# Kernel tuning notes

Measured on AMD Instinct MI355X. Metric: run time of the kernel, lower is better.

## Reference

```python
import jax, jax.numpy as jnp
import numpy as np

DIM = 512
HEADS = 8
HEAD_DIM = DIM // HEADS
SCALE = HEAD_DIM ** -0.5
GROUP1 = np.array([2, 3, 5, 6, 1, 4, 0, 7, 8, 9, 14, 15, 11, 12, 10, 13])
GROUP2 = np.array([0, 1, 2, 3, 5, 6, 4, 7])
EPS = 1e-5


def setup_inputs() -> dict:
    key = jax.random.key(0)
    ks = jax.random.split(key, 6)
    B, N, C = 4096, 16, DIM
    x = jax.random.normal(ks[0], (B, N, C), dtype=jnp.float32)
    w_q = jax.random.normal(ks[1], (C, C), dtype=jnp.float32) * 0.02
    w_kv = jax.random.normal(ks[2], (2 * C, C), dtype=jnp.float32) * 0.02
    w_proj = jax.random.normal(ks[3], (C, C), dtype=jnp.float32) * 0.02
    b_proj = jax.random.normal(ks[4], (C,), dtype=jnp.float32) * 0.02
    gamma = jnp.ones((C,), dtype=jnp.float32)
    beta = jnp.zeros((C,), dtype=jnp.float32)
    return {"x": x, "w_q": w_q, "w_kv": w_kv, "w_proj": w_proj,
            "b_proj": b_proj, "gamma": gamma, "beta": beta}


def _layernorm(x, gamma, beta):
    mu = jnp.mean(x, axis=-1, keepdims=True)
    var = jnp.mean(jnp.square(x - mu), axis=-1, keepdims=True)
    return (x - mu) * jax.lax.rsqrt(var + EPS) * gamma + beta


def _avg_pool_pairs(x):
    # x: (B, L, C) -> (B, L//2, C), AvgPool1d(kernel=2, stride=2) over L
    return 0.5 * (x[:, 0::2] + x[:, 1::2])


def reference(x, w_q, w_kv, w_proj, b_proj, gamma, beta):
    B, N, C = x.shape
    q = (x @ w_q.T).reshape(B, N, HEADS, HEAD_DIM).transpose(0, 2, 1, 3)  # (B,H,N,d)
    # gather + avgpool preprocessing
    p1 = _avg_pool_pairs(x[:, GROUP1])  # (B, 8, C)
    p2 = _avg_pool_pairs(x[:, GROUP2])  # (B, 4, C)
    pools = jnp.concatenate([x, p1, p2], axis=1)  # (B, N+12, C)
    pools = _layernorm(pools, gamma, beta)
    M = pools.shape[1]
    kv = (pools @ w_kv.T).reshape(B, M, 2, HEADS, HEAD_DIM).transpose(2, 0, 3, 1, 4)
    k, v = kv[0], kv[1]  # (B,H,M,d)
    attn = jax.nn.softmax(jnp.einsum('bhnd,bhmd->bhnm', q, k) * SCALE, axis=-1)
    out = jnp.einsum('bhnm,bhmd->bhnd', attn, v)  # (B,H,N,d)
    out = out.transpose(0, 2, 1, 3).reshape(B, N, C)
    return out @ w_proj.T + b_proj
```

## Files before the change

kernel.cpp:

```cpp
#include <hip/hip_runtime.h>
#include <hip/hip_bf16.h>
#include <cstdint>
#include <cstddef>


using bf16 = __hip_bfloat16;

#define B_SZ   4096
#define NTOK   16
#define CDIM   512
#define MPOOL  28
#define NHEAD  8
#define HDIM   64
#define LN_EPS 1e-5f
#define ATT_SCALE 0.125f

typedef short bf16x8 __attribute__((ext_vector_type(8)));
typedef float f32x4  __attribute__((ext_vector_type(4)));

__constant__ int c_g1[16] = {2,3,5,6,1,4,0,7,8,9,14,15,11,12,10,13};
__constant__ int c_g2[8]  = {0,1,2,3,5,6,4,7};

__device__ __forceinline__ unsigned short f2b(float f) {
    unsigned u = __float_as_uint(f);
    return (unsigned short)((u + 0x7FFFu + ((u >> 16) & 1u)) >> 16);
}

__device__ __forceinline__ void lds_cp16(const void* g, void* l) {
    __builtin_amdgcn_global_load_lds(
        (const __attribute__((address_space(1))) void*)g,
        (__attribute__((address_space(3))) void*)l, 16, 0, 0);
}

__global__ __launch_bounds__(256) void f32_to_bf16_kernel(
    const float* __restrict__ src, bf16* __restrict__ dst, int n8)
{
    const int i = blockIdx.x * 256 + threadIdx.x;
    if (i >= n8) return;
    const float4* p = (const float4*)(src + (size_t)i * 8);
    float4 a = p[0], b = p[1];
    uint4 pk;
    pk.x = (unsigned)f2b(a.x) | ((unsigned)f2b(a.y) << 16);
    pk.y = (unsigned)f2b(a.z) | ((unsigned)f2b(a.w) << 16);
    pk.z = (unsigned)f2b(b.x) | ((unsigned)f2b(b.y) << 16);
    pk.w = (unsigned)f2b(b.z) | ((unsigned)f2b(b.w) << 16);
    *(uint4*)(dst + (size_t)i * 8) = pk;
}

__global__ __launch_bounds__(256) void pools_ln_kernel(
    const float* __restrict__ x, const float* __restrict__ gamma,
    const float* __restrict__ beta, bf16* __restrict__ pools,
    bf16* __restrict__ xb)
{
    const int wave = threadIdx.x >> 6;
    const int lane = threadIdx.x & 63;
    const int row  = blockIdx.x * 4 + wave;
    const int b = row / MPOOL;
    const int m = row % MPOOL;
    const float* xb_src = x + (size_t)b * NTOK * CDIM;
    const int c0 = lane * 8;

    float v[8];
    if (m < 16) {
        const float4* p = (const float4*)(xb_src + m * CDIM + c0);
        float4 a = p[0], c = p[1];
        v[0]=a.x; v[1]=a.y; v[2]=a.z; v[3]=a.w;
        v[4]=c.x; v[5]=c.y; v[6]=c.z; v[7]=c.w;
        uint4 pk;
        pk.x = (unsigned)f2b(v[0]) | ((unsigned)f2b(v[1]) << 16);
        pk.y = (unsigned)f2b(v[2]) | ((unsigned)f2b(v[3]) << 16);
        pk.z = (unsigned)f2b(v[4]) | ((unsigned)f2b(v[5]) << 16);
        pk.w = (unsigned)f2b(v[6]) | ((unsigned)f2b(v[7]) << 16);
        *(uint4*)(xb + (size_t)b * NTOK * CDIM + (size_t)m * CDIM + c0) = pk;
    } else {
        int r0, r1;
        if (m < 24) { int j = m - 16; r0 = c_g1[2*j]; r1 = c_g1[2*j+1]; }
        else        { int j = m - 24; r0 = c_g2[2*j]; r1 = c_g2[2*j+1]; }
        const float4* p0 = (const float4*)(xb_src + r0 * CDIM + c0);
        const float4* p1 = (const float4*)(xb_src + r1 * CDIM + c0);
        float4 a0 = p0[0], a1 = p0[1];
        float4 b0 = p1[0], b1 = p1[1];
        v[0]=0.5f*(a0.x+b0.x); v[1]=0.5f*(a0.y+b0.y);
        v[2]=0.5f*(a0.z+b0.z); v[3]=0.5f*(a0.w+b0.w);
        v[4]=0.5f*(a1.x+b1.x); v[5]=0.5f*(a1.y+b1.y);
        v[6]=0.5f*(a1.z+b1.z); v[7]=0.5f*(a1.w+b1.w);
    }

    float s = 0.f, sq = 0.f;
#pragma unroll
    for (int j = 0; j < 8; ++j) { s += v[j]; sq += v[j]*v[j]; }
#pragma unroll
    for (int off = 1; off < 64; off <<= 1) {
        s  += __shfl_xor(s,  off, 64);
        sq += __shfl_xor(sq, off, 64);
    }
    const float mu   = s * (1.f / CDIM);
    const float var  = sq * (1.f / CDIM) - mu * mu;
    const float rstd = rsqrtf(var + LN_EPS);

    unsigned short o[8];
#pragma unroll
    for (int j = 0; j < 8; ++j) {
        float g  = gamma[c0 + j];
        float bb = beta[c0 + j];
        o[j] = f2b((v[j] - mu) * rstd * g + bb);
    }
    uint4 pk;
    pk.x = (unsigned)o[0] | ((unsigned)o[1] << 16);
    pk.y = (unsigned)o[2] | ((unsigned)o[3] << 16);
    pk.z = (unsigned)o[4] | ((unsigned)o[5] << 16);
    pk.w = (unsigned)o[6] | ((unsigned)o[7] << 16);
    *(uint4*)(pools + (size_t)row * CDIM + c0) = pk;
}

template<bool OUT_BF16, bool BIAS, int NBLK>
__global__ __launch_bounds__(512, 2) void gemm256_kernel(
    const bf16* __restrict__ A, const bf16* __restrict__ W,
    const float* __restrict__ bias, void* __restrict__ Cptr, int Ncols)
{
    constexpr int K  = 512;
    constexpr int NT = K / 32;
    extern __shared__ __align__(16) char ring[];

    const int tid = threadIdx.x;
    const int wv = tid >> 6, ln = tid & 63;
    const int wr = wv >> 2, wc = wv & 3;
    const int fr = ln & 15, kb = ln >> 4;

    const int p  = blockIdx.x;
    const int o  = p >> 3;
    const int mb = (o / NBLK) * 8 + (p & 7);
    const int nb = o % NBLK;
    const size_t m0 = (size_t)mb * 256;
    const size_t n0 = (size_t)nb * 256;

    const int srow = wv * 16 + (ln >> 2);
    const int scol = (((ln & 3) * 16) ^ (((ln >> 3) & 3) << 4)) >> 1;
    const bf16* Asrc0 = A + (m0 + srow) * K + scol;
    const bf16* Asrc1 = A + (m0 + 128 + srow) * K + scol;
    const bf16* Wsrc0 = W + (n0 + srow) * K + scol;
    const bf16* Wsrc1 = W + (n0 + 128 + srow) * K + scol;
    char* const ringc = ring;

    const int aswz  = ((fr >> 1) & 3) << 4;
    const int a_off = (wr * 128 + fr) * 64 + ((kb * 16) ^ aswz);
    const int b_off = 16384 + (wc * 64 + fr) * 64 + ((kb * 16) ^ aswz);

    f32x4 acc[8][4];
#pragma unroll
    for (int i = 0; i < 8; ++i)
#pragma unroll
    for (int j = 0; j < 4; ++j)
        acc[i][j] = f32x4{0.f, 0.f, 0.f, 0.f};

    auto STAGE = [&](int t) {
        char* base = ringc + (t & 3) * 32768 + wv * 1024;
        const int ko = t * 32;
        lds_cp16(Asrc0 + ko, base);
        lds_cp16(Asrc1 + ko, base + 8192);
        lds_cp16(Wsrc0 + ko, base + 16384);
        lds_cp16(Wsrc1 + ko, base + 16384 + 8192);
    };

    STAGE(0);
    STAGE(1);
    asm volatile("s_waitcnt vmcnt(4)" ::: "memory");
    __builtin_amdgcn_s_barrier();

#pragma unroll 1
    for (int t = 0; t < NT; ++t) {
        if (t + 2 < NT) STAGE(t + 2);
        const char* sa = ringc + (t & 3) * 32768;

        bf16x8 af[8], bfr[4];
#pragma unroll
        for (int mi = 0; mi < 8; ++mi)
            af[mi] = *(const bf16x8*)(sa + a_off + mi * 1024);
#pragma unroll
        for (int nj = 0; nj < 4; ++nj)
            bfr[nj] = *(const bf16x8*)(sa + b_off + nj * 1024);

#pragma unroll
        for (int mi = 0; mi < 8; ++mi)
#pragma unroll
        for (int nj = 0; nj < 4; ++nj)
            acc[mi][nj] = __builtin_amdgcn_mfma_f32_16x16x32_bf16(
                af[mi], bfr[nj], acc[mi][nj], 0, 0, 0);

        if (t + 2 < NT) { asm volatile("s_waitcnt vmcnt(4)" ::: "memory"); }
        else            { asm volatile("s_waitcnt vmcnt(0)" ::: "memory"); }
        __builtin_amdgcn_s_barrier();
    }

    const int orow0 = wr * 128 + kb * 4;
    const int ocol0 = wc * 64 + fr;
    float bv[4];
#pragma unroll
    for (int nj = 0; nj < 4; ++nj)
        bv[nj] = BIAS ? bias[n0 + ocol0 + nj * 16] : 0.f;
#pragma unroll
    for (int mi = 0; mi < 8; ++mi) {
        const size_t rbase = m0 + orow0 + mi * 16;
#pragma unroll
        for (int r = 0; r < 4; ++r) {
            const size_t rowoff = (rbase + r) * (size_t)Ncols + n0 + ocol0;
#pragma unroll
            for (int nj = 0; nj < 4; ++nj) {
                float v = acc[mi][nj][r] + bv[nj];
                if (OUT_BF16)
                    ((unsigned short*)Cptr)[rowoff + nj * 16] = f2b(v);
                else
                    ((float*)Cptr)[rowoff + nj * 16] = v;
            }
        }
    }
}

__global__ __launch_bounds__(512, 2) void attn_kernel(
    const bf16* __restrict__ q, const bf16* __restrict__ kv,
    bf16* __restrict__ att)
{
    extern __shared__ __align__(16) char smem[];
    char* const kvl = smem;
    unsigned short (*P_t)[512] = (unsigned short (*)[512])(smem + 65536);

    const int tid = threadIdx.x;
    const int wv = tid >> 6, ln = tid & 63;
    const int fr = ln & 15, kb = ln >> 4;
    const int b = blockIdx.x;
    const int h = wv;

    const char* kvg = (const char*)kv + (size_t)b * (MPOOL * 2 * CDIM * 2);
#pragma unroll
    for (int i = 0; i < 7; ++i) {
        const int ob  = i * 8192 + wv * 1024;
        const int row = ob >> 11;
        const int x   = ((row & 7) << 4) ^ (((row >> 3) & 3) << 5);
        const int src = ((ob & 2047) + ln * 16) ^ x;
        lds_cp16(kvg + (size_t)row * 2048 + src, kvl + ob);
    }
    *(uint4*)(kvl + 57344 + tid * 16) = uint4{0u, 0u, 0u, 0u};
    __syncthreads();

    const bf16* qb = q + (size_t)b * (NTOK * CDIM) + h * HDIM;
    bf16x8 aq[2];
#pragma unroll
    for (int ks = 0; ks < 2; ++ks)
        aq[ks] = *(const bf16x8*)(qb + fr * CDIM + ks * 32 + kb * 8);

    bf16x8 bk[2][2];
#pragma unroll
    for (int mt = 0; mt < 2; ++mt) {
        const int row = mt * 16 + fr;
        const int x   = ((row & 7) << 4) ^ (((row >> 3) & 3) << 5);
#pragma unroll
        for (int ks = 0; ks < 2; ++ks)
            bk[mt][ks] = *(const bf16x8*)(kvl + row * 2048 +
                              ((h * 128 + ks * 64 + kb * 16) ^ x));
    }

    bf16x8 bv[4];
#pragma unroll
    for (int dt = 0; dt < 4; ++dt)
#pragma unroll
        for (int j = 0; j < 8; ++j) {
            const int row = kb * 8 + j;
            const int x   = ((row & 7) << 4) ^ (((row >> 3) & 3) << 5);
            bv[dt][j] = *(const short*)(kvl + row * 2048 +
                              ((1024 + h * 128 + dt * 32 + fr * 2) ^ x));
        }

    f32x4 st0 = {0.f, 0.f, 0.f, 0.f}, st1 = {0.f, 0.f, 0.f, 0.f};
    st0 = __builtin_amdgcn_mfma_f32_16x16x32_bf16(aq[0], bk[0][0], st0, 0, 0, 0);
    st0 = __builtin_amdgcn_mfma_f32_16x16x32_bf16(aq[1], bk[0][1], st0, 0, 0, 0);
    st1 = __builtin_amdgcn_mfma_f32_16x16x32_bf16(aq[0], bk[1][0], st1, 0, 0, 0);
    st1 = __builtin_amdgcn_mfma_f32_16x16x32_bf16(aq[1], bk[1][1], st1, 0, 0, 0);

    const bool kmask = (fr >= MPOOL - 16);
#pragma unroll
    for (int r = 0; r < 4; ++r) {
        st0[r] *= ATT_SCALE;
        st1[r] = kmask ? -1e30f : st1[r] * ATT_SCALE;
    }

    float p0[4], p1[4];
#pragma unroll
    for (int r = 0; r < 4; ++r) {
        float mx = fmaxf(st0[r], st1[r]);
        mx = fmaxf(mx, __shfl_xor(mx, 1, 64));
        mx = fmaxf(mx, __shfl_xor(mx, 2, 64));
        mx = fmaxf(mx, __shfl_xor(mx, 4, 64));
        mx = fmaxf(mx, __shfl_xor(mx, 8, 64));
        float e0 = expf(st0[r] - mx);
        float e1 = expf(st1[r] - mx);
        float s = e0 + e1;
        s += __shfl_xor(s, 1, 64);
        s += __shfl_xor(s, 2, 64);
        s += __shfl_xor(s, 4, 64);
        s += __shfl_xor(s, 8, 64);
        const float inv = 1.f / s;
        p0[r] = e0 * inv;
        p1[r] = e1 * inv;
    }

    {
        ushort4 w0, w1;
        w0.x = f2b(p0[0]); w0.y = f2b(p0[1]); w0.z = f2b(p0[2]); w0.w = f2b(p0[3]);
        w1.x = f2b(p1[0]); w1.y = f2b(p1[1]); w1.z = f2b(p1[2]); w1.w = f2b(p1[3]);
        *(ushort4*)&P_t[wv][(fr)      * 16 + kb * 4] = w0;
        *(ushort4*)&P_t[wv][(16 + fr) * 16 + kb * 4] = w1;
    }
    asm volatile("s_waitcnt lgkmcnt(0)" ::: "memory");

    bf16x8 pa;
#pragma unroll
    for (int j = 0; j < 8; ++j)
        pa[j] = (short)P_t[wv][(kb * 8 + j) * 16 + fr];

    f32x4 o[4];
#pragma unroll
    for (int dt = 0; dt < 4; ++dt) {
        o[dt] = f32x4{0.f, 0.f, 0.f, 0.f};
        o[dt] = __builtin_amdgcn_mfma_f32_16x16x32_bf16(pa, bv[dt], o[dt], 0, 0, 0);
    }

    unsigned short* ob = (unsigned short*)(att + (size_t)b * (NTOK * CDIM) + h * HDIM);
#pragma unroll
    for (int r = 0; r < 4; ++r) {
        const size_t nrow = (size_t)(kb * 4 + r) * CDIM;
#pragma unroll
        for (int dt = 0; dt < 4; ++dt)
            ob[nrow + dt * 16 + fr] = f2b(o[dt][r]);
    }
}

extern "C" void kernel_launch(void* const* d_in, const int* in_sizes, int n_in,
                              void* d_out, int out_size, void* d_ws, size_t ws_size,
                              hipStream_t stream)
{
    const float* x      = (const float*)d_in[0];
    const float* w_q    = (const float*)d_in[1];
    const float* w_kv   = (const float*)d_in[2];
    const float* w_proj = (const float*)d_in[3];
    const float* b_proj = (const float*)d_in[4];
    const float* gamma  = (const float*)d_in[5];
    const float* beta   = (const float*)d_in[6];

    char* ws = (char*)d_ws;
    bf16* xb    = (bf16*)(ws);
    bf16* pools = (bf16*)(ws + 67108864ull);
    bf16* qbuf  = (bf16*)(ws + 67108864ull + 117440512ull);
    bf16* kvbuf = (bf16*)(ws + 67108864ull + 117440512ull + 67108864ull);
    bf16* wqb   = (bf16*)(ws + 67108864ull + 117440512ull + 67108864ull + 234881024ull);
    bf16* wkvb  = (bf16*)((char*)wqb + 524288ull);
    bf16* wpb   = (bf16*)((char*)wkvb + 1048576ull);
    bf16* atbuf = pools;

    hipFuncSetAttribute((const void*)gemm256_kernel<true, false, 2>,
                        hipFuncAttributeMaxDynamicSharedMemorySize, 131072);
    hipFuncSetAttribute((const void*)gemm256_kernel<true, false, 4>,
                        hipFuncAttributeMaxDynamicSharedMemorySize, 131072);
    hipFuncSetAttribute((const void*)gemm256_kernel<false, true, 2>,
                        hipFuncAttributeMaxDynamicSharedMemorySize, 131072);
    hipFuncSetAttribute((const void*)attn_kernel,
                        hipFuncAttributeMaxDynamicSharedMemorySize, 73728);

    f32_to_bf16_kernel<<<128, 256, 0, stream>>>(w_q, wqb, 32768);
    f32_to_bf16_kernel<<<256, 256, 0, stream>>>(w_kv, wkvb, 65536);
    f32_to_bf16_kernel<<<128, 256, 0, stream>>>(w_proj, wpb, 32768);

    pools_ln_kernel<<<(B_SZ * MPOOL) / 4, 256, 0, stream>>>(x, gamma, beta, pools, xb);

    gemm256_kernel<true, false, 2><<<512, 512, 131072, stream>>>(
        xb, wqb, nullptr, (void*)qbuf, 512);

    gemm256_kernel<true, false, 4><<<1792, 512, 131072, stream>>>(
        pools, wkvb, nullptr, (void*)kvbuf, 1024);

    attn_kernel<<<B_SZ, 512, 73728, stream>>>(qbuf, kvbuf, atbuf);

    gemm256_kernel<false, true, 2><<<512, 512, 131072, stream>>>(
        atbuf, wpb, b_proj, d_out, 512);
}
```

Measured before the change: 422.6 us.

## Fuse KV projection GEMM into attention kernel and merge weight conversions

Replaces the separate KV projection GEMM and attention kernels with one kernel that, per pair of batch elements, computes K and V from the pooled LayerNorm rows into LDS and then runs attention from LDS. This removes the large global round trip of the KV intermediate buffer and one launch. The three weight conversion launches are merged into a single kernel. In exchange, every block streams the full KV weight matrix from global/L2 with small M tiles and a large LDS footprint, which limits occupancy and weight reuse.

New measurement: 498.1 us. +17.9%, slower.

```diff
diff --git a/kernel.cpp b/kernel.cpp
--- a/kernel.cpp
+++ b/kernel.cpp
@@ -32,11 +32,16 @@
         (__attribute__((address_space(3))) void*)l, 16, 0, 0);
 }
 
-__global__ __launch_bounds__(256) void f32_to_bf16_kernel(
-    const float* __restrict__ src, bf16* __restrict__ dst, int n8)
+__global__ __launch_bounds__(256) void convert_all_kernel(
+    const float* __restrict__ w_q, const float* __restrict__ w_kv,
+    const float* __restrict__ w_proj, bf16* __restrict__ wqb,
+    bf16* __restrict__ wkvb, bf16* __restrict__ wpb)
 {
-    const int i = blockIdx.x * 256 + threadIdx.x;
-    if (i >= n8) return;
+    const float* src; bf16* dst; int i;
+    const int blk = blockIdx.x;
+    if (blk < 128)      { src = w_q;    dst = wqb; i = blk * 256 + threadIdx.x; }
+    else if (blk < 384) { src = w_kv;   dst = wkvb; i = (blk - 128) * 256 + threadIdx.x; }
+    else                { src = w_proj; dst = wpb; i = (blk - 384) * 256 + threadIdx.x; }
     const float4* p = (const float4*)(src + (size_t)i * 8);
     float4 a = p[0], b = p[1];
     uint4 pk;
@@ -216,121 +221,186 @@
     }
 }
 
-__global__ __launch_bounds__(512, 2) void attn_kernel(
-    const bf16* __restrict__ q, const bf16* __restrict__ kv,
-    bf16* __restrict__ att)
+__global__ __launch_bounds__(512, 2) void kvattn_kernel(
+    const bf16* __restrict__ pools, const bf16* __restrict__ wkv,
+    const bf16* __restrict__ q, bf16* __restrict__ att)
 {
     extern __shared__ __align__(16) char smem[];
-    char* const kvl = smem;
-    unsigned short (*P_t)[512] = (unsigned short (*)[512])(smem + 65536);
-
     const int tid = threadIdx.x;
     const int wv = tid >> 6, ln = tid & 63;
     const int fr = ln & 15, kb = ln >> 4;
-    const int b = blockIdx.x;
+    const int b0 = blockIdx.x * 2;
+
+    const char* Ag = (const char*)(pools + (size_t)b0 * MPOOL * CDIM);
+#pragma unroll
+    for (int i = 0; i < 8; ++i) {
+        const int row = wv * 8 + i;
+        const int x   = ((row & 7) << 4) ^ (((row >> 3) & 3) << 5);
+        lds_cp16(Ag + (size_t)row * 1024 + ((ln * 16) ^ x), smem + row * 1024);
+    }
+    __syncthreads();
+
+    const int n0w = wv * 128;
+    f32x4 acc[4][8];
+#pragma unroll
+    for (int i = 0; i < 4; ++i)
+#pragma unroll
+    for (int j = 0; j < 8; ++j)
+        acc[i][j] = f32x4{0.f, 0.f, 0.f, 0.f};
+
+    const bf16* Wl = wkv + (size_t)(n0w + fr) * CDIM + kb * 8;
+
+#pragma unroll
+    for (int t = 0; t < 16; ++t) {
+        bf16x8 bfr[8], af[4];
+#pragma unroll
+        for (int nj = 0; nj < 8; ++nj)
+            bfr[nj] = *(const bf16x8*)(Wl + (size_t)nj * 16 * CDIM + t * 32);
+#pragma unroll
+        for (int mi = 0; mi < 4; ++mi) {
+            const int row = mi * 16 + fr;
+            const int x   = ((row & 7) << 4) ^ (((row >> 3) & 3) << 5);
+            af[mi] = *(const bf16x8*)(smem + row * 1024 +
+                          ((t * 64 + kb * 16) ^ x));
+        }
+#pragma unroll
+        for (int mi = 0; mi < 4; ++mi)
+#pragma unroll
+        for (int nj = 0; nj < 8; ++nj)
+            acc[mi][nj] = __builtin_amdgcn_mfma_f32_16x16x32_bf16(
+                af[mi], bfr[nj], acc[mi][nj], 0, 0, 0);
+    }
+    __syncthreads();
+
+#pragma unroll
+    for (int mi = 0; mi < 4; ++mi) {
+#pragma unroll
+        for (int r = 0; r < 4; ++r) {
+            const int rc = mi * 16 + kb * 4 + r;
+            if (rc < 2 * MPOOL) {
+                const int bb   = (rc >= MPOOL);
+                const int m    = rc - bb * MPOOL;
+                const int lrow = bb * 32 + m;
+                const int x    = ((lrow & 7) << 4) ^ (((lrow >> 3) & 3) << 5);
+                char* dst = smem + lrow * 2048;
+#pragma unroll
+                for (int nj = 0; nj < 8; ++nj) {
+                    const int col = n0w + nj * 16 + fr;
+                    *(unsigned short*)(dst + ((col * 2) ^ x)) =
+                        f2b(acc[mi][nj][r]);
+                }
+            }
+        }
+    }
+#pragma unroll
+    for (int z = 0; z < 2; ++z) {
+        const int e    = z * 512 + tid;
+        const int rr   = e >> 7;
+        const int ro   = (e & 127) * 16;
+        const int lrow = (rr < 4) ? (28 + rr) : (56 + rr);
+        *(uint4*)(smem + lrow * 2048 + ro) = uint4{0u, 0u, 0u, 0u};
+    }
+    __syncthreads();
+
+    unsigned short* P_t = (unsigned short*)(smem + 131072) + wv * 512;
     const int h = wv;
 
-    const char* kvg = (const char*)kv + (size_t)b * (MPOOL * 2 * CDIM * 2);
-#pragma unroll
-    for (int i = 0; i < 7; ++i) {
-        const int ob  = i * 8192 + wv * 1024;
-        const int row = ob >> 11;
-        const int x   = ((row & 7) << 4) ^ (((row >> 3) & 3) << 5);
-        const int src = ((ob & 2047) + ln * 16) ^ x;
-        lds_cp16(kvg + (size_t)row * 2048 + src, kvl + ob);
-    }
-    *(uint4*)(kvl + 57344 + tid * 16) = uint4{0u, 0u, 0u, 0u};
-    __syncthreads();
-
-    const bf16* qb = q + (size_t)b * (NTOK * CDIM) + h * HDIM;
-    bf16x8 aq[2];
-#pragma unroll
-    for (int ks = 0; ks < 2; ++ks)
-        aq[ks] = *(const bf16x8*)(qb + fr * CDIM + ks * 32 + kb * 8);
-
-    bf16x8 bk[2][2];
-#pragma unroll
-    for (int mt = 0; mt < 2; ++mt) {
-        const int row = mt * 16 + fr;
-        const int x   = ((row & 7) << 4) ^ (((row >> 3) & 3) << 5);
+#pragma unroll 1
+    for (int bb = 0; bb < 2; ++bb) {
+        const char* kvl = smem + bb * 65536;
+
+        const bf16* qb = q + (size_t)(b0 + bb) * (NTOK * CDIM) + h * HDIM;
+        bf16x8 aq[2];
 #pragma unroll
         for (int ks = 0; ks < 2; ++ks)
-            bk[mt][ks] = *(const bf16x8*)(kvl + row * 2048 +
-                              ((h * 128 + ks * 64 + kb * 16) ^ x));
-    }
-
-    bf16x8 bv[4];
-#pragma unroll
-    for (int dt = 0; dt < 4; ++dt)
-#pragma unroll
-        for (int j = 0; j < 8; ++j) {
-            const int row = kb * 8 + j;
+            aq[ks] = *(const bf16x8*)(qb + fr * CDIM + ks * 32 + kb * 8);
+
+        bf16x8 bk[2][2];
+#pragma unroll
+        for (int mt = 0; mt < 2; ++mt) {
+            const int row = mt * 16 + fr;
             const int x   = ((row & 7) << 4) ^ (((row >> 3) & 3) << 5);
-            bv[dt][j] = *(const short*)(kvl + row * 2048 +
-                              ((1024 + h * 128 + dt * 32 + fr * 2) ^ x));
-        }
-
-    f32x4 st0 = {0.f, 0.f, 0.f, 0.f}, st1 = {0.f, 0.f, 0.f, 0.f};
-    st0 = __builtin_amdgcn_mfma_f32_16x16x32_bf16(aq[0], bk[0][0], st0, 0, 0, 0);
-    st0 = __builtin_amdgcn_mfma_f32_16x16x32_bf16(aq[1], bk[0][1], st0, 0, 0, 0);
-    st1 = __builtin_amdgcn_mfma_f32_16x16x32_bf16(aq[0], bk[1][0], st1, 0, 0, 0);
-    st1 = __builtin_amdgcn_mfma_f32_16x16x32_bf16(aq[1], bk[1][1], st1, 0, 0, 0);
-
-    const bool kmask = (fr >= MPOOL - 16);
-#pragma unroll
-    for (int r = 0; r < 4; ++r) {
-        st0[r] *= ATT_SCALE;
-        st1[r] = kmask ? -1e30f : st1[r] * ATT_SCALE;
-    }
-
-    float p0[4], p1[4];
-#pragma unroll
-    for (int r = 0; r < 4; ++r) {
-        float mx = fmaxf(st0[r], st1[r]);
-        mx = fmaxf(mx, __shfl_xor(mx, 1, 64));
-        mx = fmaxf(mx, __shfl_xor(mx, 2, 64));
-        mx = fmaxf(mx, __shfl_xor(mx, 4, 64));
-        mx = fmaxf(mx, __shfl_xor(mx, 8, 64));
-        float e0 = expf(st0[r] - mx);
-        float e1 = expf(st1[r] - mx);
-        float s = e0 + e1;
-        s += __shfl_xor(s, 1, 64);
-        s += __shfl_xor(s, 2, 64);
-        s += __shfl_xor(s, 4, 64);
-        s += __shfl_xor(s, 8, 64);
-        const float inv = 1.f / s;
-        p0[r] = e0 * inv;
-        p1[r] = e1 * inv;
-    }
-
-    {
-        ushort4 w0, w1;
-        w0.x = f2b(p0[0]); w0.y = f2b(p0[1]); w0.z = f2b(p0[2]); w0.w = f2b(p0[3]);
-        w1.x = f2b(p1[0]); w1.y = f2b(p1[1]); w1.z = f2b(p1[2]); w1.w = f2b(p1[3]);
-        *(ushort4*)&P_t[wv][(fr)      * 16 + kb * 4] = w0;
-        *(ushort4*)&P_t[wv][(16 + fr) * 16 + kb * 4] = w1;
-    }
-    asm volatile("s_waitcnt lgkmcnt(0)" ::: "memory");
-
-    bf16x8 pa;
-#pragma unroll
-    for (int j = 0; j < 8; ++j)
-        pa[j] = (short)P_t[wv][(kb * 8 + j) * 16 + fr];
-
-    f32x4 o[4];
-#pragma unroll
-    for (int dt = 0; dt < 4; ++dt) {
-        o[dt] = f32x4{0.f, 0.f, 0.f, 0.f};
-        o[dt] = __builtin_amdgcn_mfma_f32_16x16x32_bf16(pa, bv[dt], o[dt], 0, 0, 0);
-    }
-
-    unsigned short* ob = (unsigned short*)(att + (size_t)b * (NTOK * CDIM) + h * HDIM);
-#pragma unroll
-    for (int r = 0; r < 4; ++r) {
-        const size_t nrow = (size_t)(kb * 4 + r) * CDIM;
+#pragma unroll
+            for (int ks = 0; ks < 2; ++ks)
+                bk[mt][ks] = *(const bf16x8*)(kvl + row * 2048 +
+                                  ((h * 128 + ks * 64 + kb * 16) ^ x));
+        }
+
+        bf16x8 bv[4];
 #pragma unroll
         for (int dt = 0; dt < 4; ++dt)
-            ob[nrow + dt * 16 + fr] = f2b(o[dt][r]);
+#pragma unroll
+            for (int j = 0; j < 8; ++j) {
+                const int row = kb * 8 + j;
+                const int x   = ((row & 7) << 4) ^ (((row >> 3) & 3) << 5);
+                bv[dt][j] = *(const short*)(kvl + row * 2048 +
+                                  ((1024 + h * 128 + dt * 32 + fr * 2) ^ x));
+            }
+
+        f32x4 st0 = {0.f, 0.f, 0.f, 0.f}, st1 = {0.f, 0.f, 0.f, 0.f};
+        st0 = __builtin_amdgcn_mfma_f32_16x16x32_bf16(aq[0], bk[0][0], st0, 0, 0, 0);
+        st0 = __builtin_amdgcn_mfma_f32_16x16x32_bf16(aq[1], bk[0][1], st0, 0, 0, 0);
+        st1 = __builtin_amdgcn_mfma_f32_16x16x32_bf16(aq[0], bk[1][0], st1, 0, 0, 0);
+        st1 = __builtin_amdgcn_mfma_f32_16x16x32_bf16(aq[1], bk[1][1], st1, 0, 0, 0);
+
+        const bool kmask = (fr >= MPOOL - 16);
+#pragma unroll
+        for (int r = 0; r < 4; ++r) {
+            st0[r] *= ATT_SCALE;
+            st1[r] = kmask ? -1e30f : st1[r] * ATT_SCALE;
+        }
+
+        float p0[4], p1[4];
+#pragma unroll
+        for (int r = 0; r < 4; ++r) {
+            float mx = fmaxf(st0[r], st1[r]);
+            mx = fmaxf(mx, __shfl_xor(mx, 1, 64));
+            mx = fmaxf(mx, __shfl_xor(mx, 2, 64));
+            mx = fmaxf(mx, __shfl_xor(mx, 4, 64));
+            mx = fmaxf(mx, __shfl_xor(mx, 8, 64));
+            float e0 = expf(st0[r] - mx);
+            float e1 = expf(st1[r] - mx);
+            float s = e0 + e1;
+            s += __shfl_xor(s, 1, 64);
+            s += __shfl_xor(s, 2, 64);
+            s += __shfl_xor(s, 4, 64);
+            s += __shfl_xor(s, 8, 64);
+            const float inv = 1.f / s;
+            p0[r] = e0 * inv;
+            p1[r] = e1 * inv;
+        }
+
+        {
+            ushort4 w0, w1;
+            w0.x = f2b(p0[0]); w0.y = f2b(p0[1]); w0.z = f2b(p0[2]); w0.w = f2b(p0[3]);
+            w1.x = f2b(p1[0]); w1.y = f2b(p1[1]); w1.z = f2b(p1[2]); w1.w = f2b(p1[3]);
+            *(ushort4*)&P_t[(fr)      * 16 + kb * 4] = w0;
+            *(ushort4*)&P_t[(16 + fr) * 16 + kb * 4] = w1;
+        }
+        asm volatile("s_waitcnt lgkmcnt(0)" ::: "memory");
+
+        bf16x8 pa;
+#pragma unroll
+        for (int j = 0; j < 8; ++j)
+            pa[j] = (short)P_t[(kb * 8 + j) * 16 + fr];
+        asm volatile("s_waitcnt lgkmcnt(0)" ::: "memory");
+
+        f32x4 o[4];
+#pragma unroll
+        for (int dt = 0; dt < 4; ++dt) {
+            o[dt] = f32x4{0.f, 0.f, 0.f, 0.f};
+            o[dt] = __builtin_amdgcn_mfma_f32_16x16x32_bf16(pa, bv[dt], o[dt], 0, 0, 0);
+        }
+
+        unsigned short* ob = (unsigned short*)(att +
+            (size_t)(b0 + bb) * (NTOK * CDIM) + h * HDIM);
+#pragma unroll
+        for (int r = 0; r < 4; ++r) {
+            const size_t nrow = (size_t)(kb * 4 + r) * CDIM;
+#pragma unroll
+            for (int dt = 0; dt < 4; ++dt)
+                ob[nrow + dt * 16 + fr] = f2b(o[dt][r]);
+        }
     }
 }
 
@@ -350,35 +420,28 @@
     bf16* xb    = (bf16*)(ws);
     bf16* pools = (bf16*)(ws + 67108864ull);
     bf16* qbuf  = (bf16*)(ws + 67108864ull + 117440512ull);
-    bf16* kvbuf = (bf16*)(ws + 67108864ull + 117440512ull + 67108864ull);
     bf16* wqb   = (bf16*)(ws + 67108864ull + 117440512ull + 67108864ull + 234881024ull);
     bf16* wkvb  = (bf16*)((char*)wqb + 524288ull);
     bf16* wpb   = (bf16*)((char*)wkvb + 1048576ull);
     bf16* atbuf = pools;
+    bf16* attb  = (bf16*)(ws + 67108864ull + 117440512ull + 67108864ull + 100663296ull);
 
     hipFuncSetAttribute((const void*)gemm256_kernel<true, false, 2>,
-                        hipFuncAttributeMaxDynamicSharedMemorySize, 131072);
-    hipFuncSetAttribute((const void*)gemm256_kernel<true, false, 4>,
                         hipFuncAttributeMaxDynamicSharedMemorySize, 131072);
     hipFuncSetAttribute((const void*)gemm256_kernel<false, true, 2>,
                         hipFuncAttributeMaxDynamicSharedMemorySize, 131072);
-    hipFuncSetAttribute((const void*)attn_kernel,
-                        hipFuncAttributeMaxDynamicSharedMemorySize, 73728);
-
-    f32_to_bf16_kernel<<<128, 256, 0, stream>>>(w_q, wqb, 32768);
-    f32_to_bf16_kernel<<<256, 256, 0, stream>>>(w_kv, wkvb, 65536);
-    f32_to_bf16_kernel<<<128, 256, 0, stream>>>(w_proj, wpb, 32768);
+    hipFuncSetAttribute((const void*)kvattn_kernel,
+                        hipFuncAttributeMaxDynamicSharedMemorySize, 139264);
+
+    convert_all_kernel<<<512, 256, 0, stream>>>(w_q, w_kv, w_proj, wqb, wkvb, wpb);
 
     pools_ln_kernel<<<(B_SZ * MPOOL) / 4, 256, 0, stream>>>(x, gamma, beta, pools, xb);
 
     gemm256_kernel<true, false, 2><<<512, 512, 131072, stream>>>(
         xb, wqb, nullptr, (void*)qbuf, 512);
 
-    gemm256_kernel<true, false, 4><<<1792, 512, 131072, stream>>>(
-        pools, wkvb, nullptr, (void*)kvbuf, 1024);
-
-    attn_kernel<<<B_SZ, 512, 73728, stream>>>(qbuf, kvbuf, atbuf);
+    kvattn_kernel<<<B_SZ / 2, 512, 139264, stream>>>(pools, wkvb, qbuf, attb);
 
     gemm256_kernel<false, true, 2><<<512, 512, 131072, stream>>>(
-        atbuf, wpb, b_proj, d_out, 512);
-}
+        attb, wpb, b_proj, d_out, 512);
+}
```
